# Optimization experiments

Measured on AMD Instinct MI355X. Metric: run time of the kernel, lower is better.

The kernel has to match this reference:

```python
import jax, jax.numpy as jnp
import numpy as np

B, S, H = 2, 1024, 4096
NH, NKV, HD = 32, 8, 128
GROUPS = NH // NKV  # num_key_value_groups
ROPE_THETA = 10000.0


def setup_inputs() -> dict:
    key = jax.random.key(0)
    k0, k1, k2 = jax.random.split(key, 3)
    x = jax.random.normal(k0, (B, S, H), jnp.float32)
    w_qkv = jax.random.normal(k1, (H, (NH + 2 * NKV) * HD), jnp.float32) * (1.0 / np.sqrt(H))
    w_o = jax.random.normal(k2, (NH * HD, H), jnp.float32) * (1.0 / np.sqrt(H))
    # rotary cos/sin tables (llama freqs_cis, interleaved-pair convention)
    inv_freq = 1.0 / (ROPE_THETA ** (np.arange(0, HD, 2, dtype=np.float64) / HD))
    freqs = np.outer(np.arange(S, dtype=np.float64), inv_freq)  # [S, HD/2]
    cos = jnp.asarray(np.cos(freqs), jnp.float32)
    sin = jnp.asarray(np.sin(freqs), jnp.float32)
    # additive causal mask [1,1,S,S]
    causal = np.tril(np.ones((S, S), dtype=bool))
    mask = jnp.asarray(np.where(causal, 0.0, -1e9), jnp.float32)[None, None]
    return {"x": x, "w_qkv": w_qkv, "w_o": w_o, "cos": cos, "sin": sin, "mask": mask}


def _rope(t, cos, sin):
    # t: [B,S,N,HD]; rotate interleaved (even, odd) pairs like complex mult by freqs_cis
    t2 = t.reshape(t.shape[:-1] + (HD // 2, 2))
    t0, t1 = t2[..., 0], t2[..., 1]
    c = cos[None, :, None, :]  # [1,S,1,HD/2]
    s = sin[None, :, None, :]
    r0 = t0 * c - t1 * s
    r1 = t0 * s + t1 * c
    return jnp.stack([r0, r1], axis=-1).reshape(t.shape)


def reference(x, w_qkv, w_o, cos, sin, mask):
    b, s, _ = x.shape
    xqkv = (x @ w_qkv).reshape(b, s, NH + 2 * NKV, HD)
    xq = xqkv[:, :, :NH]                  # [b,s,NH,HD]
    xk = xqkv[:, :, NH:NH + NKV]          # [b,s,NKV,HD]
    xv = xqkv[:, :, NH + NKV:]            # [b,s,NKV,HD]
    xq = _rope(xq, cos, sin)
    xk = _rope(xk, cos, sin)
    # GQA: repeat kv heads to match query heads (repeat_interleave on head dim)
    k = jnp.repeat(xk, GROUPS, axis=2)
    v = jnp.repeat(xv, GROUPS, axis=2)
    scores = jnp.einsum('bqhd,bkhd->bhqk', xq, k) / np.float32(np.sqrt(HD))
    scores = scores + mask
    probs = jax.nn.softmax(scores.astype(jnp.float32), axis=-1).astype(xq.dtype)
    out = jnp.einsum('bhqk,bkhd->bqhd', probs, v).reshape(b, s, NH * HD)
    return out @ w_o
```

## Files before the change

### kernel.cpp

```cpp
#include <hip/hip_runtime.h>
#include <cstdint>
#include <cstddef>

typedef short bf16x8 __attribute__((ext_vector_type(8)));
typedef float f32x4 __attribute__((ext_vector_type(4)));

__device__ __forceinline__ unsigned short f2bf(float f) {
  unsigned int u = __builtin_bit_cast(unsigned int, f);
  u += 0x7fffu + ((u >> 16) & 1u);
  return (unsigned short)(u >> 16);
}

__global__ void k_convert(const float* __restrict__ in, unsigned short* __restrict__ out, int n4) {
  int i = blockIdx.x * blockDim.x + threadIdx.x;
  if (i >= n4) return;
  float4 v = ((const float4*)in)[i];
  ushort4 o;
  o.x = f2bf(v.x); o.y = f2bf(v.y); o.z = f2bf(v.z); o.w = f2bf(v.w);
  ((ushort4*)out)[i] = o;
}

__global__ void k_transpose(const float* __restrict__ src, unsigned short* __restrict__ dst,
                            int K, int N) {
  __shared__ float t[32][33];
  int n0 = blockIdx.x * 32, k0 = blockIdx.y * 32;
  int tx = threadIdx.x, ty = threadIdx.y;
#pragma unroll
  for (int i = 0; i < 4; ++i)
    t[ty * 4 + i][tx] = src[(size_t)(k0 + ty * 4 + i) * N + n0 + tx];
  __syncthreads();
#pragma unroll
  for (int i = 0; i < 4; ++i)
    dst[(size_t)(n0 + ty * 4 + i) * K + k0 + tx] = f2bf(t[tx][ty * 4 + i]);
}

template <int MODE>
__global__ __launch_bounds__(256) void k_gemm(const unsigned short* __restrict__ A,
                                              const unsigned short* __restrict__ Bt,
                                              float* __restrict__ C,
                                              unsigned short* __restrict__ Qr,
                                              unsigned short* __restrict__ Kr,
                                              unsigned short* __restrict__ Vt,
                                              const float* __restrict__ cosT,
                                              const float* __restrict__ sinT,
                                              int M, int N, int K) {
  __shared__ __align__(16) unsigned short lA[128 * 64];
  __shared__ __align__(16) unsigned short lB[128 * 64];
  const int tid = threadIdx.x;
  const int lane = tid & 63, wv = tid >> 6;
  const int wr = wv >> 1, wc = wv & 1;
  const int bm = blockIdx.x * 128, bn = blockIdx.y * 128;
  const int l16 = lane & 15, lhi = lane >> 4;
  f32x4 acc[4][4] = {};
  bf16x8 ar[4], br[4];

#pragma unroll
  for (int i = 0; i < 4; ++i) {
    int c = tid + i * 256, row = c >> 3, c16 = c & 7;
    ar[i] = *(const bf16x8*)(A + (size_t)(bm + row) * K + 0 + c16 * 8);
    br[i] = *(const bf16x8*)(Bt + (size_t)(bn + row) * K + 0 + c16 * 8);
  }
  const int nkt = K >> 6;
  for (int kt = 0; kt < nkt; ++kt) {
    __syncthreads();
#pragma unroll
    for (int i = 0; i < 4; ++i) {
      int c = tid + i * 256, row = c >> 3, c16 = c & 7;
      int pc = c16 ^ (row & 7);
      *(bf16x8*)((char*)lA + row * 128 + pc * 16) = ar[i];
      *(bf16x8*)((char*)lB + row * 128 + pc * 16) = br[i];
    }
    __syncthreads();
    if (kt + 1 < nkt) {
      int kofs = (kt + 1) << 6;
#pragma unroll
      for (int i = 0; i < 4; ++i) {
        int c = tid + i * 256, row = c >> 3, c16 = c & 7;
        ar[i] = *(const bf16x8*)(A + (size_t)(bm + row) * K + kofs + c16 * 8);
        br[i] = *(const bf16x8*)(Bt + (size_t)(bn + row) * K + kofs + c16 * 8);
      }
    }
#pragma unroll
    for (int s = 0; s < 2; ++s) {
      bf16x8 af[4], bfr[4];
#pragma unroll
      for (int f = 0; f < 4; ++f) {
        int rowa = wr * 64 + f * 16 + l16;
        int ca = (s * 4 + lhi) ^ (rowa & 7);
        af[f] = *(const bf16x8*)((char*)lA + rowa * 128 + ca * 16);
        int rowb = wc * 64 + f * 16 + l16;
        int cb = (s * 4 + lhi) ^ (rowb & 7);
        bfr[f] = *(const bf16x8*)((char*)lB + rowb * 128 + cb * 16);
      }
#pragma unroll
      for (int fi = 0; fi < 4; ++fi)
#pragma unroll
        for (int fj = 0; fj < 4; ++fj)
          acc[fi][fj] = __builtin_amdgcn_mfma_f32_16x16x32_bf16(af[fi], bfr[fj], acc[fi][fj], 0, 0, 0);
    }
  }

  if (MODE == 0) {
#pragma unroll
    for (int fi = 0; fi < 4; ++fi) {
      int rbase = bm + wr * 64 + fi * 16 + lhi * 4;
#pragma unroll
      for (int fj = 0; fj < 4; ++fj) {
        int col = bn + wc * 64 + fj * 16 + l16;
#pragma unroll
        for (int r = 0; r < 4; ++r)
          C[(size_t)(rbase + r) * N + col] = acc[fi][fj][r];
      }
    }
  } else {
#pragma unroll
    for (int fi = 0; fi < 4; ++fi) {
      int rbase = bm + wr * 64 + fi * 16 + lhi * 4;
      int b = rbase >> 10, sbase = rbase & 1023;
#pragma unroll
      for (int fj = 0; fj < 4; ++fj) {
        int col = bn + wc * 64 + fj * 16 + l16;
        if (col < 5120) {
          int i = (col & 127) >> 1;
          float sgn = (col & 1) ? 1.0f : -1.0f;
          unsigned short* dst;
          if (col < 4096)
            dst = Qr + ((size_t)(b * 32 + (col >> 7)) * 1024) * 128 + (col & 127);
          else
            dst = Kr + ((size_t)(b * 8 + ((col - 4096) >> 7)) * 1024) * 128 + (col & 127);
#pragma unroll
          for (int r = 0; r < 4; ++r) {
            float own = acc[fi][fj][r];
            float other = __shfl_xor(own, 1);
            int s = sbase + r;
            float c = cosT[s * 64 + i], sn = sinT[s * 64 + i];
            dst[(size_t)s * 128] = f2bf(own * c + sgn * other * sn);
          }
        } else {
          int kvh = (col - 5120) >> 7, d = col & 127;
          unsigned short* dst = Vt + ((size_t)(b * 8 + kvh) * 128 + d) * 1024;
#pragma unroll
          for (int r = 0; r < 4; ++r) dst[sbase + r] = f2bf(acc[fi][fj][r]);
        }
      }
    }
  }
}

__global__ __launch_bounds__(256) void k_attn(const unsigned short* __restrict__ Qr,
                                              const unsigned short* __restrict__ Kr,
                                              const unsigned short* __restrict__ Vt,
                                              unsigned short* __restrict__ Out) {
  __shared__ __align__(16) unsigned short lK[64 * 128];
  __shared__ __align__(16) unsigned short lV[128 * 64];
  __shared__ __align__(16) unsigned short lP[4 * 16 * 64];
  const int tid = threadIdx.x, lane = tid & 63, wv = tid >> 6;
  const int qt = blockIdx.x, h = blockIdx.y, b = blockIdx.z;
  const int kvh = h >> 2;
  const int q0 = qt * 64;
  const int l16 = lane & 15, lhi = lane >> 4;

  const unsigned short* Qbase = Qr + ((size_t)(b * 32 + h) * 1024 + q0 + wv * 16 + l16) * 128;
  bf16x8 qf[4];
#pragma unroll
  for (int s = 0; s < 4; ++s) qf[s] = *(const bf16x8*)(Qbase + s * 32 + lhi * 8);

  const unsigned short* Kbase = Kr + (size_t)(b * 8 + kvh) * 1024 * 128;
  const unsigned short* Vbase = Vt + (size_t)(b * 8 + kvh) * 128 * 1024;

  f32x4 oacc[8] = {};
  float mrow[4] = {-1e30f, -1e30f, -1e30f, -1e30f};
  float lrow[4] = {0.f, 0.f, 0.f, 0.f};
  const int ntk = qt + 1;
  bf16x8 kreg[4], vreg[4];

#pragma unroll
  for (int i = 0; i < 4; ++i) {
    int c = tid + i * 256;
    int krow = c >> 4, kc = c & 15;
    kreg[i] = *(const bf16x8*)(Kbase + (size_t)krow * 128 + kc * 8);
    int vrow = c >> 3, vc = c & 7;
    vreg[i] = *(const bf16x8*)(Vbase + (size_t)vrow * 1024 + vc * 8);
  }

  for (int kt = 0; kt < ntk; ++kt) {
    const int k0 = kt * 64;
    __syncthreads();
#pragma unroll
    for (int i = 0; i < 4; ++i) {
      int c = tid + i * 256;
      int krow = c >> 4, kc = c & 15;
      *(bf16x8*)((char*)lK + krow * 256 + (kc ^ (krow & 7)) * 16) = kreg[i];
      int vrow = c >> 3, vc = c & 7;
      *(bf16x8*)((char*)lV + vrow * 128 + (vc ^ (vrow & 7)) * 16) = vreg[i];
    }
    __syncthreads();

    if (kt + 1 < ntk) {
      const int kn = (kt + 1) * 64;
#pragma unroll
      for (int i = 0; i < 4; ++i) {
        int c = tid + i * 256;
        int krow = c >> 4, kc = c & 15;
        kreg[i] = *(const bf16x8*)(Kbase + (size_t)(kn + krow) * 128 + kc * 8);
        int vrow = c >> 3, vc = c & 7;
        vreg[i] = *(const bf16x8*)(Vbase + (size_t)vrow * 1024 + kn + vc * 8);
      }
    }

    f32x4 sacc[4] = {};
#pragma unroll
    for (int kf = 0; kf < 4; ++kf) {
      int rowk = kf * 16 + l16;
#pragma unroll
      for (int s = 0; s < 4; ++s) {
        int ck = (s * 4 + lhi) ^ (rowk & 7);
        bf16x8 kfr = *(const bf16x8*)((char*)lK + rowk * 256 + ck * 16);
        sacc[kf] = __builtin_amdgcn_mfma_f32_16x16x32_bf16(qf[s], kfr, sacc[kf], 0, 0, 0);
      }
    }

    const int qg = q0 + wv * 16 + lhi * 4;
    float mt[4] = {-1e30f, -1e30f, -1e30f, -1e30f};
#pragma unroll
    for (int kf = 0; kf < 4; ++kf) {
      int kg = k0 + kf * 16 + l16;
#pragma unroll
      for (int r = 0; r < 4; ++r) {
        float v = sacc[kf][r] * 0.08838834764831845f;
        v = (kg <= qg + r) ? v : -1e9f;
        sacc[kf][r] = v;
        mt[r] = fmaxf(mt[r], v);
      }
    }
#pragma unroll
    for (int r = 0; r < 4; ++r) {
#pragma unroll
      for (int off = 1; off < 16; off <<= 1) mt[r] = fmaxf(mt[r], __shfl_xor(mt[r], off));
    }
    float alpha[4], rs[4];
#pragma unroll
    for (int r = 0; r < 4; ++r) {
      float mn = fmaxf(mrow[r], mt[r]);
      alpha[r] = __expf(mrow[r] - mn);
      mrow[r] = mn;
      rs[r] = 0.f;
    }
#pragma unroll
    for (int kf = 0; kf < 4; ++kf) {
      int key = kf * 16 + l16;
#pragma unroll
      for (int r = 0; r < 4; ++r) {
        float p = __expf(sacc[kf][r] - mrow[r]);
        rs[r] += p;
        int prow = lhi * 4 + r;
        int addr = wv * 2048 + ((prow * 128 + key * 2) ^ ((prow & 7) << 4));
        *(unsigned short*)((char*)lP + addr) = f2bf(p);
      }
    }
#pragma unroll
    for (int r = 0; r < 4; ++r) {
#pragma unroll
      for (int off = 1; off < 16; off <<= 1) rs[r] += __shfl_xor(rs[r], off);
      lrow[r] = lrow[r] * alpha[r] + rs[r];
    }
#pragma unroll
    for (int nf = 0; nf < 8; ++nf)
#pragma unroll
      for (int r = 0; r < 4; ++r) oacc[nf][r] *= alpha[r];

#pragma unroll
    for (int s2 = 0; s2 < 2; ++s2) {
      int prow = l16;
      int paddr = wv * 2048 + ((prow * 128 + s2 * 64 + lhi * 16) ^ ((prow & 7) << 4));
      bf16x8 pa = *(const bf16x8*)((char*)lP + paddr);
#pragma unroll
      for (int nf = 0; nf < 8; ++nf) {
        int rowd = nf * 16 + l16;
        int cv = (s2 * 4 + lhi) ^ (rowd & 7);
        bf16x8 vfr = *(const bf16x8*)((char*)lV + rowd * 128 + cv * 16);
        oacc[nf] = __builtin_amdgcn_mfma_f32_16x16x32_bf16(pa, vfr, oacc[nf], 0, 0, 0);
      }
    }
  }

  unsigned short* Ob = Out + ((size_t)(b * 1024) + q0 + wv * 16 + lhi * 4) * 4096 + h * 128;
#pragma unroll
  for (int r = 0; r < 4; ++r) {
    float inv = 1.f / lrow[r];
#pragma unroll
    for (int nf = 0; nf < 8; ++nf)
      Ob[(size_t)r * 4096 + nf * 16 + l16] = f2bf(oacc[nf][r] * inv);
  }
}

extern "C" void kernel_launch(void* const* d_in, const int* in_sizes, int n_in,
                              void* d_out, int out_size, void* d_ws, size_t ws_size,
                              hipStream_t stream) {
  const float* x = (const float*)d_in[0];
  const float* w_qkv = (const float*)d_in[1];
  const float* w_o = (const float*)d_in[2];
  const float* cosT = (const float*)d_in[3];
  const float* sinT = (const float*)d_in[4];

  char* ws = (char*)d_ws;
  unsigned short* wqkv_t = (unsigned short*)(ws);
  unsigned short* wo_t   = (unsigned short*)(ws + 50331648);
  unsigned short* xb     = (unsigned short*)(ws + 83886080);
  unsigned short* Qr     = (unsigned short*)(ws + 100663296);
  unsigned short* Kr     = (unsigned short*)(ws + 117440512);
  unsigned short* Vt     = (unsigned short*)(ws + 121634816);
  unsigned short* attn   = (unsigned short*)(ws + 125829120);

  k_convert<<<8192, 256, 0, stream>>>(x, xb, 2048 * 4096 / 4);
  k_transpose<<<dim3(6144 / 32, 4096 / 32), dim3(32, 8), 0, stream>>>(w_qkv, wqkv_t, 4096, 6144);
  k_transpose<<<dim3(4096 / 32, 4096 / 32), dim3(32, 8), 0, stream>>>(w_o, wo_t, 4096, 4096);
  k_gemm<1><<<dim3(16, 48), 256, 0, stream>>>(xb, wqkv_t, nullptr, Qr, Kr, Vt, cosT, sinT,
                                              2048, 6144, 4096);
  k_attn<<<dim3(16, 32, 2), 256, 0, stream>>>(Qr, Kr, Vt, attn);
  k_gemm<0><<<dim3(16, 32), 256, 0, stream>>>(attn, wo_t, (float*)d_out, nullptr, nullptr, nullptr,
                                              nullptr, nullptr, 2048, 4096, 4096);
}
```

Before: 332.7 us.

## Double-buffer GEMM LDS tiles and prefetch two K-tiles ahead

Splits the GEMM's LDS staging into two buffers and keeps two register sets of global loads in flight, so each K-step needs one barrier instead of two and global loads run two tiles ahead of compute. The goal is to hide global-memory latency and cut synchronisation inside the main GEMM loop. The cost is doubled LDS use (64 KB per block) and more vector registers, which can lower occupancy. It also assumes the K-tile count is even.

```diff
diff --git a/kernel.cpp b/kernel.cpp
--- a/kernel.cpp
+++ b/kernel.cpp
@@ -44,42 +44,34 @@
                                               const float* __restrict__ cosT,
                                               const float* __restrict__ sinT,
                                               int M, int N, int K) {
-  __shared__ __align__(16) unsigned short lA[128 * 64];
-  __shared__ __align__(16) unsigned short lB[128 * 64];
+  __shared__ __align__(16) unsigned short lA[2][128 * 64];
+  __shared__ __align__(16) unsigned short lB[2][128 * 64];
   const int tid = threadIdx.x;
   const int lane = tid & 63, wv = tid >> 6;
   const int wr = wv >> 1, wc = wv & 1;
   const int bm = blockIdx.x * 128, bn = blockIdx.y * 128;
   const int l16 = lane & 15, lhi = lane >> 4;
   f32x4 acc[4][4] = {};
-  bf16x8 ar[4], br[4];
-
-#pragma unroll
-  for (int i = 0; i < 4; ++i) {
-    int c = tid + i * 256, row = c >> 3, c16 = c & 7;
-    ar[i] = *(const bf16x8*)(A + (size_t)(bm + row) * K + 0 + c16 * 8);
-    br[i] = *(const bf16x8*)(Bt + (size_t)(bn + row) * K + 0 + c16 * 8);
-  }
-  const int nkt = K >> 6;
-  for (int kt = 0; kt < nkt; ++kt) {
-    __syncthreads();
+  bf16x8 a0[4], b0[4], a1[4], b1[4];
+
+  auto loadT = [&](int kofs, bf16x8 (&ar)[4], bf16x8 (&br)[4]) {
+#pragma unroll
+    for (int i = 0; i < 4; ++i) {
+      int c = tid + i * 256, row = c >> 3, c16 = c & 7;
+      ar[i] = *(const bf16x8*)(A + (size_t)(bm + row) * K + kofs + c16 * 8);
+      br[i] = *(const bf16x8*)(Bt + (size_t)(bn + row) * K + kofs + c16 * 8);
+    }
+  };
+  auto writeT = [&](int buf, bf16x8 (&ar)[4], bf16x8 (&br)[4]) {
 #pragma unroll
     for (int i = 0; i < 4; ++i) {
       int c = tid + i * 256, row = c >> 3, c16 = c & 7;
       int pc = c16 ^ (row & 7);
-      *(bf16x8*)((char*)lA + row * 128 + pc * 16) = ar[i];
-      *(bf16x8*)((char*)lB + row * 128 + pc * 16) = br[i];
-    }
-    __syncthreads();
-    if (kt + 1 < nkt) {
-      int kofs = (kt + 1) << 6;
-#pragma unroll
-      for (int i = 0; i < 4; ++i) {
-        int c = tid + i * 256, row = c >> 3, c16 = c & 7;
-        ar[i] = *(const bf16x8*)(A + (size_t)(bm + row) * K + kofs + c16 * 8);
-        br[i] = *(const bf16x8*)(Bt + (size_t)(bn + row) * K + kofs + c16 * 8);
-      }
-    }
+      *(bf16x8*)((char*)lA[buf] + row * 128 + pc * 16) = ar[i];
+      *(bf16x8*)((char*)lB[buf] + row * 128 + pc * 16) = br[i];
+    }
+  };
+  auto computeT = [&](int buf) {
 #pragma unroll
     for (int s = 0; s < 2; ++s) {
       bf16x8 af[4], bfr[4];
@@ -87,10 +79,10 @@
       for (int f = 0; f < 4; ++f) {
         int rowa = wr * 64 + f * 16 + l16;
         int ca = (s * 4 + lhi) ^ (rowa & 7);
-        af[f] = *(const bf16x8*)((char*)lA + rowa * 128 + ca * 16);
+        af[f] = *(const bf16x8*)((char*)lA[buf] + rowa * 128 + ca * 16);
         int rowb = wc * 64 + f * 16 + l16;
         int cb = (s * 4 + lhi) ^ (rowb & 7);
-        bfr[f] = *(const bf16x8*)((char*)lB + rowb * 128 + cb * 16);
+        bfr[f] = *(const bf16x8*)((char*)lB[buf] + rowb * 128 + cb * 16);
       }
 #pragma unroll
       for (int fi = 0; fi < 4; ++fi)
@@ -98,6 +90,20 @@
         for (int fj = 0; fj < 4; ++fj)
           acc[fi][fj] = __builtin_amdgcn_mfma_f32_16x16x32_bf16(af[fi], bfr[fj], acc[fi][fj], 0, 0, 0);
     }
+  };
+
+  loadT(0, a0, b0);
+  loadT(64, a1, b1);
+  const int nkt = K >> 6;
+  for (int kt = 0; kt < nkt; kt += 2) {
+    writeT(0, a0, b0);
+    __syncthreads();
+    if (kt + 2 < nkt) loadT((kt + 2) << 6, a0, b0);
+    computeT(0);
+    writeT(1, a1, b1);
+    __syncthreads();
+    if (kt + 3 < nkt) loadT((kt + 3) << 6, a1, b1);
+    computeT(1);
   }
 
   if (MODE == 0) {
```

New measurement: 333.1 us. About the same (+0.1%).
